# Performance work log

Hardware: AMD Instinct MI355X
Metric: run time of the kernel (lower is better)

Reference implementation:

```python
import jax, jax.numpy as jnp
import numpy as np

SCALING = 10.0  # init kwarg 'scaling'
EPS = 1e-12


def setup_inputs() -> dict:
    key = jax.random.key(0)
    k1, k2, k3 = jax.random.split(key, 3)
    N, d, n_classes = 512, 256, 32
    feat = jax.random.normal(k1, (N, d), dtype=jnp.float32)
    logits = jax.random.normal(k2, (N, n_classes), dtype=jnp.float32)  # unused by the loss
    y = jax.random.randint(k3, (N,), 0, n_classes, dtype=jnp.int32)
    return {"feat": feat, "logits": logits, "y": y}


def reference(feat, logits, y):
    # Pairwise Euclidean distances D[i, j] = ||feat_i - feat_j||_2 (torch.pdist equivalent,
    # expanded to a full square matrix instead of condensed form + python index gymnastics).
    sq_norms = jnp.sum(feat * feat, axis=-1)                       # [N]
    sq = sq_norms[:, None] + sq_norms[None, :] - 2.0 * (feat @ feat.T)
    D = jnp.sqrt(jnp.maximum(sq, EPS))                             # [N, N]

    # BatchAll triplet validity masks (replaces the O(N^3) python loop):
    # (a, p): y_a == y_p and a != p ; (a, n): y_n != y_a.
    same = y[:, None] == y[None, :]                                # [N, N]
    n = y.shape[0]
    pos_mask = same & ~jnp.eye(n, dtype=bool)                      # [N, N]
    neg_mask = ~same                                               # [N, N]
    tri_mask = pos_mask[:, :, None] & neg_mask[:, None, :]         # [N, N, N]

    # loss per triplet = sigmoid(scaling * (d_pos - d_neg)); mean over valid triplets
    delta = D[:, :, None] - D[:, None, :]                          # [N, N, N]
    losses = jax.nn.sigmoid(SCALING * delta)
    total = jnp.sum(jnp.where(tri_mask, losses, 0.0))
    count = jnp.sum(tri_mask).astype(feat.dtype)
    return total / count  # size_average=True -> mean over triplets
```

## Files before the change

kernel.cpp:

```cpp
#include <hip/hip_runtime.h>
#include <math.h>

#define N 512
#define DIM 256
#define NBLK 256
#define APB 2
#define SCALING 10.0f
#define EPS 1e-12f

__global__ __launch_bounds__(NBLK) void anchor_kernel(
    const float* __restrict__ feat, const int* __restrict__ y,
    float* __restrict__ block_sum, float* __restrict__ block_cnt)
{
    __shared__ float fa[APB][DIM];
    __shared__ int   ysh[N];
    __shared__ float pos_d[APB][N];
    __shared__ float neg_d[APB][N];
    __shared__ int   n_pos[APB], n_neg[APB];
    __shared__ float red[NBLK / 64];

    const int a0  = blockIdx.x * APB;
    const int tid = threadIdx.x;

    #pragma unroll
    for (int q = 0; q < APB; ++q)
        fa[q][tid] = feat[(a0 + q) * DIM + tid];
    ysh[tid]       = y[tid];
    ysh[tid + 256] = y[tid + 256];
    if (tid < APB) { n_pos[tid] = 0; n_neg[tid] = 0; }
    __syncthreads();

    const int ya0 = ysh[a0];
    const int ya1 = ysh[a0 + 1];

    const float4* feat4 = reinterpret_cast<const float4*>(feat);
    #pragma unroll
    for (int r = 0; r < 2; ++r) {
        const int j = tid + r * 256;
        const float4* rowj = feat4 + j * (DIM / 4);
        float acc0 = 0.0f, acc1 = 0.0f;
        #pragma unroll 8
        for (int k = 0; k < DIM / 4; ++k) {
            float4 v = rowj[k];
            float e0, e1, e2, e3;
            e0 = v.x - fa[0][4 * k + 0];
            e1 = v.y - fa[0][4 * k + 1];
            e2 = v.z - fa[0][4 * k + 2];
            e3 = v.w - fa[0][4 * k + 3];
            acc0 += e0 * e0 + e1 * e1 + e2 * e2 + e3 * e3;
            e0 = v.x - fa[1][4 * k + 0];
            e1 = v.y - fa[1][4 * k + 1];
            e2 = v.z - fa[1][4 * k + 2];
            e3 = v.w - fa[1][4 * k + 3];
            acc1 += e0 * e0 + e1 * e1 + e2 * e2 + e3 * e3;
        }
        const float d0 = sqrtf(fmaxf(acc0, EPS));
        const float d1 = sqrtf(fmaxf(acc1, EPS));
        const int yj = ysh[j];
        if (yj == ya0) {
            if (j != a0) { int i = atomicAdd(&n_pos[0], 1); pos_d[0][i] = d0; }
        } else {
            int i = atomicAdd(&n_neg[0], 1); neg_d[0][i] = d0;
        }
        if (yj == ya1) {
            if (j != a0 + 1) { int i = atomicAdd(&n_pos[1], 1); pos_d[1][i] = d1; }
        } else {
            int i = atomicAdd(&n_neg[1], 1); neg_d[1][i] = d1;
        }
    }
    __syncthreads();

    float acc = 0.0f;
    int   cnt = 0;
    #pragma unroll
    for (int q = 0; q < APB; ++q) {
        const int np = n_pos[q];
        const int nn = n_neg[q];
        cnt += np * nn;
        for (int p = 0; p < np; ++p) {
            const float dp = pos_d[q][p];
            for (int n = tid; n < nn; n += NBLK) {
                float x = SCALING * (dp - neg_d[q][n]);
                acc += 1.0f / (1.0f + __expf(-x));
            }
        }
    }

    #pragma unroll
    for (int s = 32; s > 0; s >>= 1)
        acc += __shfl_down(acc, s, 64);
    if ((tid & 63) == 0) red[tid >> 6] = acc;
    __syncthreads();
    if (tid == 0) {
        float t = red[0] + red[1] + red[2] + red[3];
        block_sum[blockIdx.x] = t;
        block_cnt[blockIdx.x] = (float)cnt;
    }
}

__global__ __launch_bounds__(NBLK) void finalize_kernel(
    const float* __restrict__ block_sum, const float* __restrict__ block_cnt,
    float* __restrict__ out)
{
    __shared__ double s_sum[NBLK];
    __shared__ double s_cnt[NBLK];
    const int tid = threadIdx.x;
    s_sum[tid] = (double)block_sum[tid];
    s_cnt[tid] = (double)block_cnt[tid];
    __syncthreads();
    for (int s = NBLK / 2; s > 0; s >>= 1) {
        if (tid < s) {
            s_sum[tid] += s_sum[tid + s];
            s_cnt[tid] += s_cnt[tid + s];
        }
        __syncthreads();
    }
    if (tid == 0) out[0] = (float)(s_sum[0] / s_cnt[0]);
}

extern "C" void kernel_launch(void* const* d_in, const int* in_sizes, int n_in,
                              void* d_out, int out_size, void* d_ws, size_t ws_size,
                              hipStream_t stream) {
    const float* feat = (const float*)d_in[0];
    const int* y = (const int*)d_in[2];

    float* block_sum = (float*)d_ws;
    float* block_cnt = block_sum + (N / APB);
    float* out = (float*)d_out;

    anchor_kernel<<<N / APB, NBLK, 0, stream>>>(feat, y, block_sum, block_cnt);
    finalize_kernel<<<1, NBLK, 0, stream>>>(block_sum, block_cnt, out);
}
```

Measured before the change: 84.55 us.

## Fuse finalize into triplet kernel via last-block reduction and ballot compaction

Merges the finalize kernel into the main kernel using an atomic done-counter so the last block performs the global reduction, and adds a memset in place of the second launch. Block size doubles to 512 so each thread computes one row's distances, and anchor rows are read directly from global memory instead of being staged in shared memory. Per-thread shared atomics for compaction are replaced by wave ballot, popcount and a single atomic per wave. The scaling factor is folded into the distances so the sigmoid needs one fewer multiply. The memset still costs a launch, and the loss over negatives now runs with 512 threads over about 496 negatives, which leaves some threads idle.

```diff
diff --git a/kernel.cpp b/kernel.cpp
--- a/kernel.cpp
+++ b/kernel.cpp
@@ -1,72 +1,92 @@
 #include <hip/hip_runtime.h>
 #include <math.h>
 
-#define N 512
-#define DIM 256
-#define NBLK 256
-#define APB 2
-#define SCALING 10.0f
-#define EPS 1e-12f
+#define N        512
+#define DIM      256
+#define NTHR     512
+#define APB      2
+#define NBLOCKS  (N / APB)
+#define SCALING  10.0f
+#define EPS      1e-12f
 
-__global__ __launch_bounds__(NBLK) void anchor_kernel(
+__global__ __launch_bounds__(NTHR) void triplet_kernel(
     const float* __restrict__ feat, const int* __restrict__ y,
-    float* __restrict__ block_sum, float* __restrict__ block_cnt)
+    float* __restrict__ block_sum, float* __restrict__ block_cnt,
+    unsigned int* __restrict__ done_ctr, float* __restrict__ out)
 {
-    __shared__ float fa[APB][DIM];
-    __shared__ int   ysh[N];
-    __shared__ float pos_d[APB][N];
-    __shared__ float neg_d[APB][N];
-    __shared__ int   n_pos[APB], n_neg[APB];
-    __shared__ float red[NBLK / 64];
+    __shared__ float  pos_d[APB][N];
+    __shared__ float  neg_d[APB][N];
+    __shared__ int    n_pos[APB], n_neg[APB];
+    __shared__ float  red_s[NTHR / 64];
+    __shared__ double fin_s[NBLOCKS];
+    __shared__ double fin_c[NBLOCKS];
+    __shared__ int    lastflag;
 
-    const int a0  = blockIdx.x * APB;
-    const int tid = threadIdx.x;
+    const int tid  = threadIdx.x;
+    const int bid  = blockIdx.x;
+    const int a0   = bid * APB;
+    const int lane = tid & 63;
 
-    #pragma unroll
-    for (int q = 0; q < APB; ++q)
-        fa[q][tid] = feat[(a0 + q) * DIM + tid];
-    ysh[tid]       = y[tid];
-    ysh[tid + 256] = y[tid + 256];
     if (tid < APB) { n_pos[tid] = 0; n_neg[tid] = 0; }
     __syncthreads();
 
-    const int ya0 = ysh[a0];
-    const int ya1 = ysh[a0 + 1];
+    const float4* f4   = reinterpret_cast<const float4*>(feat);
+    const float4* rowj = f4 + tid * (DIM / 4);
+    const float4* ra0  = f4 + a0 * (DIM / 4);
+    const float4* ra1  = ra0 + (DIM / 4);
+    float acc0 = 0.0f, acc1 = 0.0f;
+    #pragma unroll 8
+    for (int k = 0; k < DIM / 4; ++k) {
+        const float4 v  = rowj[k];
+        const float4 u0 = ra0[k];
+        const float4 u1 = ra1[k];
+        float e;
+        e = v.x - u0.x; acc0 += e * e;
+        e = v.y - u0.y; acc0 += e * e;
+        e = v.z - u0.z; acc0 += e * e;
+        e = v.w - u0.w; acc0 += e * e;
+        e = v.x - u1.x; acc1 += e * e;
+        e = v.y - u1.y; acc1 += e * e;
+        e = v.z - u1.z; acc1 += e * e;
+        e = v.w - u1.w; acc1 += e * e;
+    }
+    const float d0 = SCALING * sqrtf(fmaxf(acc0, EPS));
+    const float d1 = SCALING * sqrtf(fmaxf(acc1, EPS));
 
-    const float4* feat4 = reinterpret_cast<const float4*>(feat);
-    #pragma unroll
-    for (int r = 0; r < 2; ++r) {
-        const int j = tid + r * 256;
-        const float4* rowj = feat4 + j * (DIM / 4);
-        float acc0 = 0.0f, acc1 = 0.0f;
-        #pragma unroll 8
-        for (int k = 0; k < DIM / 4; ++k) {
-            float4 v = rowj[k];
-            float e0, e1, e2, e3;
-            e0 = v.x - fa[0][4 * k + 0];
-            e1 = v.y - fa[0][4 * k + 1];
-            e2 = v.z - fa[0][4 * k + 2];
-            e3 = v.w - fa[0][4 * k + 3];
-            acc0 += e0 * e0 + e1 * e1 + e2 * e2 + e3 * e3;
-            e0 = v.x - fa[1][4 * k + 0];
-            e1 = v.y - fa[1][4 * k + 1];
-            e2 = v.z - fa[1][4 * k + 2];
-            e3 = v.w - fa[1][4 * k + 3];
-            acc1 += e0 * e0 + e1 * e1 + e2 * e2 + e3 * e3;
+    const int yj  = y[tid];
+    const int ya0 = y[a0];
+    const int ya1 = y[a0 + 1];
+
+    const unsigned long long below = (1ull << lane) - 1ull;
+    {
+        const bool ip  = (yj == ya0) & (tid != a0);
+        const bool ineg = (yj != ya0);
+        const unsigned long long mp = __ballot(ip);
+        const unsigned long long mn = __ballot(ineg);
+        int bp = 0, bn = 0;
+        if (lane == 0) {
+            bp = atomicAdd(&n_pos[0], (int)__popcll(mp));
+            bn = atomicAdd(&n_neg[0], (int)__popcll(mn));
         }
-        const float d0 = sqrtf(fmaxf(acc0, EPS));
-        const float d1 = sqrtf(fmaxf(acc1, EPS));
-        const int yj = ysh[j];
-        if (yj == ya0) {
-            if (j != a0) { int i = atomicAdd(&n_pos[0], 1); pos_d[0][i] = d0; }
-        } else {
-            int i = atomicAdd(&n_neg[0], 1); neg_d[0][i] = d0;
+        bp = __shfl(bp, 0, 64);
+        bn = __shfl(bn, 0, 64);
+        if (ip)   pos_d[0][bp + (int)__popcll(mp & below)] = d0;
+        if (ineg) neg_d[0][bn + (int)__popcll(mn & below)] = d0;
+    }
+    {
+        const bool ip  = (yj == ya1) & (tid != a0 + 1);
+        const bool ineg = (yj != ya1);
+        const unsigned long long mp = __ballot(ip);
+        const unsigned long long mn = __ballot(ineg);
+        int bp = 0, bn = 0;
+        if (lane == 0) {
+            bp = atomicAdd(&n_pos[1], (int)__popcll(mp));
+            bn = atomicAdd(&n_neg[1], (int)__popcll(mn));
         }
-        if (yj == ya1) {
-            if (j != a0 + 1) { int i = atomicAdd(&n_pos[1], 1); pos_d[1][i] = d1; }
-        } else {
-            int i = atomicAdd(&n_neg[1], 1); neg_d[1][i] = d1;
-        }
+        bp = __shfl(bp, 0, 64);
+        bn = __shfl(bn, 0, 64);
+        if (ip)   pos_d[1][bp + (int)__popcll(mp & below)] = d1;
+        if (ineg) neg_d[1][bn + (int)__popcll(mn & below)] = d1;
     }
     __syncthreads();
 
@@ -79,9 +99,9 @@
         cnt += np * nn;
         for (int p = 0; p < np; ++p) {
             const float dp = pos_d[q][p];
-            for (int n = tid; n < nn; n += NBLK) {
-                float x = SCALING * (dp - neg_d[q][n]);
-                acc += 1.0f / (1.0f + __expf(-x));
+            for (int n = tid; n < nn; n += NTHR) {
+                const float e = __expf(neg_d[q][n] - dp);
+                acc += __fdividef(1.0f, 1.0f + e);
             }
         }
     }
@@ -89,33 +109,35 @@
     #pragma unroll
     for (int s = 32; s > 0; s >>= 1)
         acc += __shfl_down(acc, s, 64);
-    if ((tid & 63) == 0) red[tid >> 6] = acc;
+    if (lane == 0) red_s[tid >> 6] = acc;
     __syncthreads();
+
     if (tid == 0) {
-        float t = red[0] + red[1] + red[2] + red[3];
-        block_sum[blockIdx.x] = t;
-        block_cnt[blockIdx.x] = (float)cnt;
+        float t = 0.0f;
+        #pragma unroll
+        for (int w = 0; w < NTHR / 64; ++w) t += red_s[w];
+        __hip_atomic_store(&block_sum[bid], t, __ATOMIC_RELAXED, __HIP_MEMORY_SCOPE_AGENT);
+        __hip_atomic_store(&block_cnt[bid], (float)cnt, __ATOMIC_RELAXED, __HIP_MEMORY_SCOPE_AGENT);
+        const unsigned int prev =
+            __hip_atomic_fetch_add(done_ctr, 1u, __ATOMIC_ACQ_REL, __HIP_MEMORY_SCOPE_AGENT);
+        lastflag = (prev == NBLOCKS - 1) ? 1 : 0;
     }
-}
+    __syncthreads();
 
-__global__ __launch_bounds__(NBLK) void finalize_kernel(
-    const float* __restrict__ block_sum, const float* __restrict__ block_cnt,
-    float* __restrict__ out)
-{
-    __shared__ double s_sum[NBLK];
-    __shared__ double s_cnt[NBLK];
-    const int tid = threadIdx.x;
-    s_sum[tid] = (double)block_sum[tid];
-    s_cnt[tid] = (double)block_cnt[tid];
-    __syncthreads();
-    for (int s = NBLK / 2; s > 0; s >>= 1) {
-        if (tid < s) {
-            s_sum[tid] += s_sum[tid + s];
-            s_cnt[tid] += s_cnt[tid + s];
+    if (lastflag) {
+        if (tid < NBLOCKS) {
+            const float s = __hip_atomic_load(&block_sum[tid], __ATOMIC_RELAXED, __HIP_MEMORY_SCOPE_AGENT);
+            const float c = __hip_atomic_load(&block_cnt[tid], __ATOMIC_RELAXED, __HIP_MEMORY_SCOPE_AGENT);
+            fin_s[tid] = (double)s;
+            fin_c[tid] = (double)c;
         }
         __syncthreads();
+        for (int st = NBLOCKS / 2; st > 0; st >>= 1) {
+            if (tid < st) { fin_s[tid] += fin_s[tid + st]; fin_c[tid] += fin_c[tid + st]; }
+            __syncthreads();
+        }
+        if (tid == 0) out[0] = (float)(fin_s[0] / fin_c[0]);
     }
-    if (tid == 0) out[0] = (float)(s_sum[0] / s_cnt[0]);
 }
 
 extern "C" void kernel_launch(void* const* d_in, const int* in_sizes, int n_in,
@@ -125,9 +147,10 @@
     const int* y = (const int*)d_in[2];
 
     float* block_sum = (float*)d_ws;
-    float* block_cnt = block_sum + (N / APB);
-    float* out = (float*)d_out;
+    float* block_cnt = block_sum + NBLOCKS;
+    unsigned int* done_ctr = (unsigned int*)(block_cnt + NBLOCKS);
 
-    anchor_kernel<<<N / APB, NBLK, 0, stream>>>(feat, y, block_sum, block_cnt);
-    finalize_kernel<<<1, NBLK, 0, stream>>>(block_sum, block_cnt, out);
+    hipMemsetAsync(done_ctr, 0, sizeof(unsigned int), stream);
+    triplet_kernel<<<NBLOCKS, NTHR, 0, stream>>>(feat, y, block_sum, block_cnt,
+                                                 done_ctr, (float*)d_out);
 }
```

Result: faster. 81.00 us (-4.2%).
